# Kernel tuning notes

Measured on AMD Instinct MI355X. Metric: run time of the kernel, lower is better.

The kernel has to match this reference:

```python
import jax, jax.numpy as jnp
import numpy as np

B, N, D, H, FF, K, L = 8, 4096, 128, 8, 512, 16, 2
DH = D // H
EPS = 1e-5


def setup_inputs() -> dict:
    key = jax.random.key(0)
    ks = jax.random.split(key, 32)
    s = 0.02
    inp = {
        "x": jax.random.normal(ks[0], (B, N, 8), dtype=jnp.float32),
        "xyz_w": jax.random.normal(ks[1], (D, 3), jnp.float32) * s,
        "xyz_b": jnp.zeros((D,), jnp.float32),
        "ohe_w": jax.random.normal(ks[2], (D, 5), jnp.float32) * s,
        "ohe_b": jnp.zeros((D,), jnp.float32),
        # per-layer transformer params stacked on leading L axis
        "in_proj_w": jax.random.normal(ks[3], (L, 3 * D, D), jnp.float32) * s,
        "in_proj_b": jnp.zeros((L, 3 * D), jnp.float32),
        "out_proj_w": jax.random.normal(ks[4], (L, D, D), jnp.float32) * s,
        "out_proj_b": jnp.zeros((L, D), jnp.float32),
        "ln1_w": jnp.ones((L, D), jnp.float32),
        "ln1_b": jnp.zeros((L, D), jnp.float32),
        "lin1_w": jax.random.normal(ks[5], (L, FF, D), jnp.float32) * s,
        "lin1_b": jnp.zeros((L, FF), jnp.float32),
        "lin2_w": jax.random.normal(ks[6], (L, D, FF), jnp.float32) * s,
        "lin2_b": jnp.zeros((L, D), jnp.float32),
        "ln2_w": jnp.ones((L, D), jnp.float32),
        "ln2_b": jnp.zeros((L, D), jnp.float32),
        "fc1_w": jax.random.normal(ks[7], (FF, D), jnp.float32) * s,
        "fc1_b": jnp.zeros((FF,), jnp.float32),
        "fc2_w": jax.random.normal(ks[8], (1, FF), jnp.float32) * s,
        "fc2_b": jnp.zeros((1,), jnp.float32),
    }
    return inp


def _layer_norm(x, w, b):
    m = jnp.mean(x, -1, keepdims=True)
    v = jnp.mean((x - m) ** 2, -1, keepdims=True)
    return (x - m) * jax.lax.rsqrt(v + EPS) * w + b


def _knn_attention(xyz, feat):
    # squared euclidean distances preserve top-k ordering of cdist(p=2)
    d2 = jnp.sum((xyz[:, :, None, :] - xyz[:, None, :, :]) ** 2, -1)  # [B,N,N]
    _, idx = jax.lax.top_k(-d2, K + 1)  # ascending distance
    idx = idx[..., 1:]  # drop self -> [B,N,K]
    knn = jax.vmap(lambda f, i: f[i])(feat, idx)  # [B,N,K,D]
    scale = 1.0 / np.sqrt(D)
    scores = jnp.einsum('bnd,bnkd->bnk', feat, knn) * scale
    w = jax.nn.softmax(scores, -1)
    return jnp.einsum('bnk,bnkd->bnd', w, knn)


def _mha(x, in_w, in_b, out_w, out_b):
    qkv = x @ in_w.T + in_b  # [B,N,3D]
    q, k, v = jnp.split(qkv, 3, axis=-1)
    def heads(t):
        return t.reshape(B, N, H, DH).transpose(0, 2, 1, 3)  # [B,H,N,DH]
    q, k, v = heads(q), heads(k), heads(v)
    scores = jnp.einsum('bhqd,bhkd->bhqk', q, k) / np.sqrt(DH)
    a = jax.nn.softmax(scores, -1)
    o = jnp.einsum('bhqk,bhkd->bhqd', a, v).transpose(0, 2, 1, 3).reshape(B, N, D)
    return o @ out_w.T + out_b


def reference(x, xyz_w, xyz_b, ohe_w, ohe_b, in_proj_w, in_proj_b, out_proj_w,
              out_proj_b, ln1_w, ln1_b, lin1_w, lin1_b, lin2_w, lin2_b,
              ln2_w, ln2_b, fc1_w, fc1_b, fc2_w, fc2_b):
    xyz = x[:, :, :3]
    ohe = x[:, :, 3:8]
    feat = (xyz @ xyz_w.T + xyz_b) + (ohe @ ohe_w.T + ohe_b)  # [B,N,D]
    h = _knn_attention(xyz, feat)
    # post-norm TransformerEncoder (PyTorch default, relu, no dropout at eval)
    for l in range(L):
        a = _mha(h, in_proj_w[l], in_proj_b[l], out_proj_w[l], out_proj_b[l])
        h = _layer_norm(h + a, ln1_w[l], ln1_b[l])
        f = jax.nn.relu(h @ lin1_w[l].T + lin1_b[l]) @ lin2_w[l].T + lin2_b[l]
        h = _layer_norm(h + f, ln2_w[l], ln2_b[l])
    pooled = jnp.mean(h, axis=1)  # [B,D]
    out = jax.nn.sigmoid(jax.nn.relu(pooled @ fc1_w.T + fc1_b) @ fc2_w.T + fc2_b)
    return out
```

## Files before the change

### kernel.cpp

```cpp
#include <hip/hip_runtime.h>

#define Bq 8
#define Nq 4096
#define Dq 128
#define Hq 8
#define FFq 512
#define KNNq 16
#define Lq 2
#define DHq 16
#define EPSq 1e-5f

typedef _Float16 half4 __attribute__((ext_vector_type(4)));
typedef _Float16 half2t __attribute__((ext_vector_type(2)));
typedef float v4f __attribute__((ext_vector_type(4)));

static __device__ __forceinline__ half2t pkrtz(float a, float b) {
    return __builtin_bit_cast(half2t, __builtin_amdgcn_cvt_pkrtz(a, b));
}

__global__ void wcvt_kernel(const float* __restrict__ ipw, const float* __restrict__ opw,
                            const float* __restrict__ l1w, const float* __restrict__ l2w,
                            _Float16* __restrict__ wb) {
    int i = blockIdx.x * 256 + threadIdx.x;
    float v;
    if (i < 98304) v = ipw[i];
    else if (i < 131072) v = opw[i - 98304];
    else if (i < 262144) v = l1w[i - 131072];
    else v = l2w[i - 262144];
    wb[i] = (_Float16)v;
}

__global__ void feat_kernel(const float* __restrict__ x, const float* __restrict__ xyz_w,
                            const float* __restrict__ xyz_b, const float* __restrict__ ohe_w,
                            const float* __restrict__ ohe_b, _Float16* __restrict__ feat16) {
    int i = blockIdx.x * blockDim.x + threadIdx.x;
    if (i >= Bq * Nq * Dq) return;
    int d = i & 127;
    int t = i >> 7;
    const float* xr = x + (size_t)t * 8;
    float s = xyz_b[d] + ohe_b[d];
    s += xr[0] * xyz_w[d * 3 + 0] + xr[1] * xyz_w[d * 3 + 1] + xr[2] * xyz_w[d * 3 + 2];
    s += xr[3] * ohe_w[d * 5 + 0] + xr[4] * ohe_w[d * 5 + 1] + xr[5] * ohe_w[d * 5 + 2]
       + xr[6] * ohe_w[d * 5 + 3] + xr[7] * ohe_w[d * 5 + 4];
    feat16[i] = (_Float16)s;
}

__global__ __launch_bounds__(256) void knn_kernel(const float* __restrict__ x, int* __restrict__ idx) {
    __shared__ __attribute__((aligned(16))) float sxyz[Nq][4];
    __shared__ unsigned int md[256][16];
    int b = blockIdx.y;
    int tid = threadIdx.x;
    for (int p = tid; p < Nq; p += 256) {
        const float* xr = x + ((size_t)b * Nq + p) * 8;
        float4 v = make_float4(xr[0], xr[1], xr[2], 0.f);
        *(float4*)&sxyz[p][0] = v;
    }
    __syncthreads();
    int qi = tid >> 3;
    int part = tid & 7;
    int n = blockIdx.x * 32 + qi;
    float qx = sxyz[n][0], qy = sxyz[n][1], qz = sxyz[n][2];
    unsigned int bd[KNNq];
#pragma unroll
    for (int i = 0; i < KNNq; i++) bd[i] = 0xFFFFFFFFu;
    int j0 = part * 512;
    int rot = part * 2;
#pragma unroll 2
    for (int jj = 0; jj < 512; jj++) {
        int j = j0 + ((jj + rot) & 511);
        float4 p4 = *(const float4*)&sxyz[j][0];
        float dx = qx - p4.x, dy = qy - p4.y, dz = qz - p4.z;
        float d2 = fmaf(dx, dx, fmaf(dy, dy, dz * dz));
        unsigned int key = (__float_as_uint(d2) & 0xFFFFF000u) | (unsigned int)j;
        key = (j == n) ? 0xFFFFFFFFu : key;
#pragma unroll
        for (int i = 0; i < KNNq; i++) {
            unsigned int lo = bd[i] < key ? bd[i] : key;
            unsigned int hi = bd[i] < key ? key : bd[i];
            bd[i] = lo; key = hi;
        }
    }
#pragma unroll
    for (int i = 0; i < KNNq; i++) md[tid][i] = bd[i];
    __syncthreads();
    if (part == 0) {
        unsigned int pall = 0;
        int* op = idx + ((size_t)b * Nq + n) * KNNq;
        int base_row = qi * 8;
#pragma unroll
        for (int s = 0; s < KNNq; s++) {
            unsigned int best = 0xFFFFFFFFu; int bp = 0;
#pragma unroll
            for (int p2 = 0; p2 < 8; p2++) {
                unsigned int ptr = (pall >> (p2 * 4)) & 15u;
                unsigned int v = md[base_row + p2][ptr];
                if (v < best) { best = v; bp = p2; }
            }
            op[s] = (int)(best & 4095u);
            pall += (1u << (bp * 4));
        }
    }
}

__global__ __launch_bounds__(256, 4) void knn_attn_kernel(const _Float16* __restrict__ feat16,
                                                          const int* __restrict__ idx,
                                                          float* __restrict__ h,
                                                          _Float16* __restrict__ h16) {
    int wave = threadIdx.x >> 6;
    int lane = threadIdx.x & 63;
    int token = blockIdx.x * 4 + wave;
    int b = token >> 12;
    half2t fh = ((const half2t*)(feat16 + (size_t)token * Dq))[lane];
    float2 f = make_float2((float)fh[0], (float)fh[1]);
    const int* ip = idx + (size_t)token * KNNq;
    int jj[KNNq];
#pragma unroll
    for (int k = 0; k < KNNq; k++) jj[k] = ip[k];
    float2 g[KNNq];
#pragma unroll
    for (int k = 0; k < KNNq; k++) {
        half2t gh = ((const half2t*)(feat16 + (((size_t)b << 12) + jj[k]) * Dq))[lane];
        g[k] = make_float2((float)gh[0], (float)gh[1]);
    }
    float sc[KNNq];
#pragma unroll
    for (int k = 0; k < KNNq; k++) {
        float p = f.x * g[k].x + f.y * g[k].y;
#pragma unroll
        for (int m = 1; m < 64; m <<= 1) p += __shfl_xor(p, m);
        sc[k] = p * 0.088388347648318447f;
    }
    float mx = sc[0];
#pragma unroll
    for (int k = 1; k < KNNq; k++) mx = fmaxf(mx, sc[k]);
    float sum = 0.f;
#pragma unroll
    for (int k = 0; k < KNNq; k++) { sc[k] = __expf(sc[k] - mx); sum += sc[k]; }
    float inv = 1.f / sum;
    float o0 = 0.f, o1 = 0.f;
#pragma unroll
    for (int k = 0; k < KNNq; k++) { o0 += sc[k] * g[k].x; o1 += sc[k] * g[k].y; }
    o0 *= inv; o1 *= inv;
    ((float2*)(h + (size_t)token * Dq))[lane] = make_float2(o0, o1);
    ((half2t*)(h16 + (size_t)token * Dq))[lane] = pkrtz(o0, o1);
}

template <int MODE>
__global__ __launch_bounds__(256) void hgemm_kernel(const _Float16* __restrict__ A,
                                                    const _Float16* __restrict__ W,
                                                    const float* __restrict__ bias,
                                                    void* __restrict__ Cout,
                                                    int M, int Nc, int K) {
    int tid = threadIdx.x;
    int lane = tid & 63, w = tid >> 6;
    int l15 = lane & 15, l4 = lane >> 4;
    int m0 = blockIdx.y * 64 + w * 16;
    int n0 = blockIdx.x * 64;
    const _Float16* Ap = A + (size_t)(m0 + l15) * K + l4 * 4;
    const _Float16* Wp = W + (size_t)(n0 + l15) * K + l4 * 4;
    v4f acc[4] = {{0.f, 0.f, 0.f, 0.f}, {0.f, 0.f, 0.f, 0.f}, {0.f, 0.f, 0.f, 0.f}, {0.f, 0.f, 0.f, 0.f}};
    for (int ks = 0; ks < K; ks += 16) {
        half4 af = *(const half4*)(Ap + ks);
#pragma unroll
        for (int nt = 0; nt < 4; nt++) {
            half4 wf = *(const half4*)(Wp + (size_t)nt * 16 * K + ks);
            acc[nt] = __builtin_amdgcn_mfma_f32_16x16x16f16(wf, af, acc[nt], 0, 0, 0);
        }
    }
    int m = m0 + l15;
#pragma unroll
    for (int nt = 0; nt < 4; nt++) {
        int nb = n0 + nt * 16 + l4 * 4;
        float4 bv = *(const float4*)(bias + nb);
        float v0 = acc[nt][0] + bv.x, v1 = acc[nt][1] + bv.y;
        float v2 = acc[nt][2] + bv.z, v3 = acc[nt][3] + bv.w;
        if (MODE == 1) {
            v0 = fmaxf(v0, 0.f); v1 = fmaxf(v1, 0.f); v2 = fmaxf(v2, 0.f); v3 = fmaxf(v3, 0.f);
        }
        int n_base = n0 + nt * 16;
        int sel = n_base >> 7;
        if (MODE == 2 && sel == 0) {
            v0 *= 0.36067376f; v1 *= 0.36067376f; v2 *= 0.36067376f; v3 *= 0.36067376f;
        }
        half2t lo = pkrtz(v0, v1);
        half2t hi = pkrtz(v2, v3);
        half4 hv; hv[0] = lo[0]; hv[1] = lo[1]; hv[2] = hi[0]; hv[3] = hi[1];
        if (MODE == 1) {
            *(half4*)((_Float16*)Cout + (size_t)m * Nc + nb) = hv;
        } else {
            if (sel < 2) {
                int hh = (n_base >> 4) & 7;
                size_t base = (size_t)sel * (64ull * Nq * 16)
                            + ((size_t)((m >> 12) * 8 + hh)) * (Nq * 16)
                            + (size_t)(m & 4095) * 16 + l4 * 4;
                *(half4*)((_Float16*)Cout + base) = hv;
            } else {
                int hh = (n_base >> 4) & 7;
                size_t vb = 2ull * 64 * Nq * 16
                          + ((size_t)((m >> 12) * 8 + hh)) * (16 * Nq)
                          + (size_t)(m & 4095);
                _Float16* vp = (_Float16*)Cout + vb + (size_t)(l4 * 4) * Nq;
                vp[0 * Nq] = hv[0]; vp[1 * Nq] = hv[1]; vp[2 * Nq] = hv[2]; vp[3 * Nq] = hv[3];
            }
        }
    }
}

__global__ __launch_bounds__(256) void flash7_kernel(const _Float16* __restrict__ pk,
                                                     _Float16* __restrict__ out16) {
    __shared__ _Float16 Ks[2][64 * 20];
    __shared__ _Float16 Vs[2][16 * 66];
    int tid = threadIdx.x;
    int lane = tid & 63, w = tid >> 6;
    int bh = blockIdx.y;
    const _Float16* Qb = pk + (size_t)bh * (Nq * 16);
    const _Float16* Kb = pk + (size_t)(64 + bh) * (Nq * 16);
    const _Float16* Vt = pk + 2ull * 64 * Nq * 16 + (size_t)bh * (16 * Nq);
    int q0 = blockIdx.x * 64 + w * 16;
    int l15 = lane & 15, l4 = lane >> 4;

    half4 qf = *(const half4*)(Qb + (size_t)(q0 + l15) * 16 + l4 * 4);
    half4 ones; ones[0] = (_Float16)1.f; ones[1] = (_Float16)1.f; ones[2] = (_Float16)1.f; ones[3] = (_Float16)1.f;

    int sr = tid >> 2, sc = tid & 3;
    int vd = tid >> 4, vj = (tid & 15) * 4;
    const _Float16* Kg = Kb + (size_t)sr * 16 + sc * 4;
    const _Float16* Vg = Vt + (size_t)vd * Nq + vj;

    *(half4*)(Ks[0] + sr * 20 + sc * 4) = *(const half4*)(Kg);
    *(half4*)(Vs[0] + vd * 66 + vj) = *(const half4*)(Vg);
    __syncthreads();

    v4f o = {0.f, 0.f, 0.f, 0.f};
    v4f ls = {0.f, 0.f, 0.f, 0.f};

    for (int kt = 0; kt < Nq / 64; kt++) {
        int cur = kt & 1, nxt = cur ^ 1;
        if (kt < Nq / 64 - 1) {
            *(half4*)(Ks[nxt] + sr * 20 + sc * 4) = *(const half4*)(Kg + (size_t)(kt + 1) * 64 * 16);
            *(half4*)(Vs[nxt] + vd * 66 + vj) = *(const half4*)(Vg + (kt + 1) * 64);
        }
        v4f S[4];
#pragma unroll
        for (int g = 0; g < 4; g++) {
            half4 kf = *(const half4*)(Ks[cur] + (g * 16 + l15) * 20 + l4 * 4);
            S[g] = __builtin_amdgcn_mfma_f32_16x16x16f16(kf, qf, (v4f){0.f, 0.f, 0.f, 0.f}, 0, 0, 0);
        }
        half4 P[4];
#pragma unroll
        for (int g = 0; g < 4; g++) {
            float p0 = __builtin_amdgcn_exp2f(S[g][0]);
            float p1 = __builtin_amdgcn_exp2f(S[g][1]);
            float p2 = __builtin_amdgcn_exp2f(S[g][2]);
            float p3 = __builtin_amdgcn_exp2f(S[g][3]);
            half2t lo = pkrtz(p0, p1);
            half2t hi = pkrtz(p2, p3);
            P[g][0] = lo[0]; P[g][1] = lo[1]; P[g][2] = hi[0]; P[g][3] = hi[1];
        }
#pragma unroll
        for (int g = 0; g < 4; g++) {
            half4 vf = *(const half4*)(Vs[cur] + l15 * 66 + g * 16 + l4 * 4);
            o = __builtin_amdgcn_mfma_f32_16x16x16f16(vf, P[g], o, 0, 0, 0);
            ls = __builtin_amdgcn_mfma_f32_16x16x16f16(ones, P[g], ls, 0, 0, 0);
        }
        __syncthreads();
    }
    float inv = 1.f / ls[0];
    int row = q0 + l15;
    int b = bh >> 3, hh = bh & 7;
    half2t lo = pkrtz(o[0] * inv, o[1] * inv);
    half2t hi = pkrtz(o[2] * inv, o[3] * inv);
    half4 hv; hv[0] = lo[0]; hv[1] = lo[1]; hv[2] = hi[0]; hv[3] = hi[1];
    *(half4*)(out16 + ((size_t)(b * Nq + row)) * Dq + hh * 16 + l4 * 4) = hv;
}

__global__ __launch_bounds__(256) void hgemm_ln_kernel(const _Float16* __restrict__ A,
                                                       const _Float16* __restrict__ W,
                                                       const float* __restrict__ bias,
                                                       const float* __restrict__ lnw,
                                                       const float* __restrict__ lnb,
                                                       float* __restrict__ h,
                                                       _Float16* __restrict__ h16,
                                                       int K) {
    int tid = threadIdx.x;
    int lane = tid & 63, w = tid >> 6;
    int l15 = lane & 15, l4 = lane >> 4;
    int m0 = blockIdx.x * 64 + w * 16;
    const _Float16* Ap = A + (size_t)(m0 + l15) * K + l4 * 4;
    const _Float16* Wp = W + (size_t)l15 * K + l4 * 4;
    v4f acc[8] = {};
    for (int ks = 0; ks < K; ks += 16) {
        half4 af = *(const half4*)(Ap + ks);
#pragma unroll
        for (int nt = 0; nt < 8; nt++) {
            half4 wf = *(const half4*)(Wp + (size_t)nt * 16 * K + ks);
            acc[nt] = __builtin_amdgcn_mfma_f32_16x16x16f16(wf, af, acc[nt], 0, 0, 0);
        }
    }
    int m = m0 + l15;
    float x[8][4];
    float psum = 0.f;
#pragma unroll
    for (int nt = 0; nt < 8; nt++) {
        int nb = nt * 16 + l4 * 4;
        float4 bv = *(const float4*)(bias + nb);
        half4 rv = *(const half4*)(h16 + (size_t)m * Dq + nb);
        x[nt][0] = acc[nt][0] + bv.x + (float)rv[0];
        x[nt][1] = acc[nt][1] + bv.y + (float)rv[1];
        x[nt][2] = acc[nt][2] + bv.z + (float)rv[2];
        x[nt][3] = acc[nt][3] + bv.w + (float)rv[3];
        psum += (x[nt][0] + x[nt][1]) + (x[nt][2] + x[nt][3]);
    }
    psum += __shfl_xor(psum, 16);
    psum += __shfl_xor(psum, 32);
    float mean = psum * (1.f / 128.f);
    float vsum = 0.f;
#pragma unroll
    for (int nt = 0; nt < 8; nt++)
#pragma unroll
        for (int r = 0; r < 4; r++) {
            x[nt][r] -= mean;
            vsum += x[nt][r] * x[nt][r];
        }
    vsum += __shfl_xor(vsum, 16);
    vsum += __shfl_xor(vsum, 32);
    float inv = rsqrtf(vsum * (1.f / 128.f) + EPSq);
#pragma unroll
    for (int nt = 0; nt < 8; nt++) {
        int nb = nt * 16 + l4 * 4;
        float4 wv = *(const float4*)(lnw + nb);
        float4 bb = *(const float4*)(lnb + nb);
        float y0 = x[nt][0] * inv * wv.x + bb.x;
        float y1 = x[nt][1] * inv * wv.y + bb.y;
        float y2 = x[nt][2] * inv * wv.z + bb.z;
        float y3 = x[nt][3] * inv * wv.w + bb.w;
        *(float4*)(h + (size_t)m * Dq + nb) = make_float4(y0, y1, y2, y3);
        half2t lo = pkrtz(y0, y1);
        half2t hi = pkrtz(y2, y3);
        half4 hv2; hv2[0] = lo[0]; hv2[1] = lo[1]; hv2[2] = hi[0]; hv2[3] = hi[1];
        *(half4*)(h16 + (size_t)m * Dq + nb) = hv2;
    }
}

__global__ void pool_kernel(const float* __restrict__ h, float* __restrict__ part) {
    int c = blockIdx.x, b = blockIdx.y, d = threadIdx.x;
    const float* p = h + ((size_t)b * Nq + c * 256) * Dq + d;
    float s = 0.f;
    for (int n = 0; n < 256; n++) s += p[(size_t)n * Dq];
    part[((size_t)b * 16 + c) * Dq + d] = s;
}

__global__ __launch_bounds__(512) void head_kernel(const float* __restrict__ part,
                                                   const float* __restrict__ fc1_w, const float* __restrict__ fc1_b,
                                                   const float* __restrict__ fc2_w, const float* __restrict__ fc2_b,
                                                   float* __restrict__ out) {
    __shared__ float psh[Dq];
    __shared__ float red[512];
    int b = blockIdx.x, f = threadIdx.x;
    if (f < Dq) {
        float s = 0.f;
        for (int c = 0; c < 16; c++) s += part[((size_t)b * 16 + c) * Dq + f];
        psh[f] = s * (1.f / 4096.f);
    }
    __syncthreads();
    const float* wr = fc1_w + (size_t)f * Dq;
    float s = fc1_b[f];
    for (int d = 0; d < Dq; d++) s += psh[d] * wr[d];
    red[f] = fmaxf(s, 0.f) * fc2_w[f];
    __syncthreads();
    for (int st = 256; st > 0; st >>= 1) {
        if (f < st) red[f] += red[f + st];
        __syncthreads();
    }
    if (f == 0) out[b] = 1.f / (1.f + __expf(-(red[0] + fc2_b[0])));
}

extern "C" void kernel_launch(void* const* d_in, const int* in_sizes, int n_in,
                              void* d_out, int out_size, void* d_ws, size_t ws_size,
                              hipStream_t stream) {
    const float* x        = (const float*)d_in[0];
    const float* xyz_w    = (const float*)d_in[1];
    const float* xyz_b    = (const float*)d_in[2];
    const float* ohe_w    = (const float*)d_in[3];
    const float* ohe_b    = (const float*)d_in[4];
    const float* in_proj_w  = (const float*)d_in[5];
    const float* in_proj_b  = (const float*)d_in[6];
    const float* out_proj_w = (const float*)d_in[7];
    const float* out_proj_b = (const float*)d_in[8];
    const float* ln1_w    = (const float*)d_in[9];
    const float* ln1_b    = (const float*)d_in[10];
    const float* lin1_w   = (const float*)d_in[11];
    const float* lin1_b   = (const float*)d_in[12];
    const float* lin2_w   = (const float*)d_in[13];
    const float* lin2_b   = (const float*)d_in[14];
    const float* ln2_w    = (const float*)d_in[15];
    const float* ln2_b    = (const float*)d_in[16];
    const float* fc1_w    = (const float*)d_in[17];
    const float* fc1_b    = (const float*)d_in[18];
    const float* fc2_w    = (const float*)d_in[19];
    const float* fc2_b    = (const float*)d_in[20];
    float* outp = (float*)d_out;

    char* ws = (char*)d_ws;
    size_t off = 0;
    auto alloc = [&](size_t bytes) { void* p = ws + off; off += (bytes + 255) & ~255ULL; return p; };
    _Float16*  feat16 = (_Float16*)alloc((size_t)Bq * Nq * Dq * 2);
    float*     h      = (float*)alloc((size_t)Bq * Nq * Dq * 4);
    _Float16*  h16    = (_Float16*)alloc((size_t)Bq * Nq * Dq * 2);
    _Float16*  abuf16 = (_Float16*)alloc((size_t)Bq * Nq * Dq * 2);
    char*      bigu   = (char*)alloc((size_t)Bq * Nq * FFq * 2);
    _Float16*  wb     = (_Float16*)alloc(393216ull * 2);
    int*       idx    = (int*)alloc((size_t)Bq * Nq * KNNq * 4);
    float*     part   = (float*)alloc((size_t)Bq * 16 * Dq * 4);
    if (off > ws_size) return;
    _Float16* pkb   = (_Float16*)bigu;
    _Float16* big16 = (_Float16*)bigu;

    const _Float16* wip16 = wb;
    const _Float16* wop16 = wb + 98304;
    const _Float16* wl116 = wb + 131072;
    const _Float16* wl216 = wb + 262144;

    int M = Bq * Nq;

    wcvt_kernel<<<1536, 256, 0, stream>>>(in_proj_w, out_proj_w, lin1_w, lin2_w, wb);
    feat_kernel<<<(Bq * Nq * Dq + 255) / 256, 256, 0, stream>>>(x, xyz_w, xyz_b, ohe_w, ohe_b, feat16);
    knn_kernel<<<dim3(Nq / 32, Bq), 256, 0, stream>>>(x, idx);
    knn_attn_kernel<<<M / 4, 256, 0, stream>>>(feat16, idx, h, h16);

    for (int l = 0; l < Lq; l++) {
        hgemm_kernel<2><<<dim3(384 / 64, M / 64), 256, 0, stream>>>(
            h16, wip16 + (size_t)l * 384 * 128, in_proj_b + l * 384, pkb, M, 384, 128);
        flash7_kernel<<<dim3(Nq / 64, Bq * Hq), 256, 0, stream>>>(pkb, abuf16);
        hgemm_ln_kernel<<<M / 64, 256, 0, stream>>>(
            abuf16, wop16 + (size_t)l * 128 * 128, out_proj_b + l * 128,
            ln1_w + l * 128, ln1_b + l * 128, h, h16, 128);
        hgemm_kernel<1><<<dim3(512 / 64, M / 64), 256, 0, stream>>>(
            h16, wl116 + (size_t)l * 512 * 128, lin1_b + l * 512, big16, M, 512, 128);
        hgemm_ln_kernel<<<M / 64, 256, 0, stream>>>(
            big16, wl216 + (size_t)l * 128 * 512, lin2_b + l * 128,
            ln2_w + l * 128, ln2_b + l * 128, h, h16, 512);
    }

    pool_kernel<<<dim3(16, Bq), 128, 0, stream>>>(h, part);
    head_kernel<<<Bq, 512, 0, stream>>>(part, fc1_w, fc1_b, fc2_w, fc2_b, outp);
}
```

Before: 1.161 ms.

## Fuse FFN lin1, ReLU, lin2 and LayerNorm into one register-resident kernel

Adds an ffn_kernel where each wave computes lin1 plus ReLU for its 16 rows and keeps the 512-wide fp16 intermediate in registers. It then runs lin2, the residual add and LayerNorm in the same kernel. This removes the round trip of the large intermediate activation buffer through global memory and one kernel launch per layer. The workspace now allocates only the qkv pack buffer, and the unused ReLU path in hgemm_kernel is dropped. In exchange each wave holds many more VGPRs, which may lower occupancy, and it still streams both weight matrices from cache without LDS reuse.

```diff
diff --git a/kernel.cpp b/kernel.cpp
--- a/kernel.cpp
+++ b/kernel.cpp
@@ -174,9 +174,6 @@
         float4 bv = *(const float4*)(bias + nb);
         float v0 = acc[nt][0] + bv.x, v1 = acc[nt][1] + bv.y;
         float v2 = acc[nt][2] + bv.z, v3 = acc[nt][3] + bv.w;
-        if (MODE == 1) {
-            v0 = fmaxf(v0, 0.f); v1 = fmaxf(v1, 0.f); v2 = fmaxf(v2, 0.f); v3 = fmaxf(v3, 0.f);
-        }
         int n_base = n0 + nt * 16;
         int sel = n_base >> 7;
         if (MODE == 2 && sel == 0) {
@@ -185,23 +182,19 @@
         half2t lo = pkrtz(v0, v1);
         half2t hi = pkrtz(v2, v3);
         half4 hv; hv[0] = lo[0]; hv[1] = lo[1]; hv[2] = hi[0]; hv[3] = hi[1];
-        if (MODE == 1) {
-            *(half4*)((_Float16*)Cout + (size_t)m * Nc + nb) = hv;
+        if (sel < 2) {
+            int hh = (n_base >> 4) & 7;
+            size_t base = (size_t)sel * (64ull * Nq * 16)
+                        + ((size_t)((m >> 12) * 8 + hh)) * (Nq * 16)
+                        + (size_t)(m & 4095) * 16 + l4 * 4;
+            *(half4*)((_Float16*)Cout + base) = hv;
         } else {
-            if (sel < 2) {
-                int hh = (n_base >> 4) & 7;
-                size_t base = (size_t)sel * (64ull * Nq * 16)
-                            + ((size_t)((m >> 12) * 8 + hh)) * (Nq * 16)
-                            + (size_t)(m & 4095) * 16 + l4 * 4;
-                *(half4*)((_Float16*)Cout + base) = hv;
-            } else {
-                int hh = (n_base >> 4) & 7;
-                size_t vb = 2ull * 64 * Nq * 16
-                          + ((size_t)((m >> 12) * 8 + hh)) * (16 * Nq)
-                          + (size_t)(m & 4095);
-                _Float16* vp = (_Float16*)Cout + vb + (size_t)(l4 * 4) * Nq;
-                vp[0 * Nq] = hv[0]; vp[1 * Nq] = hv[1]; vp[2 * Nq] = hv[2]; vp[3 * Nq] = hv[3];
-            }
+            int hh = (n_base >> 4) & 7;
+            size_t vb = 2ull * 64 * Nq * 16
+                      + ((size_t)((m >> 12) * 8 + hh)) * (16 * Nq)
+                      + (size_t)(m & 4095);
+            _Float16* vp = (_Float16*)Cout + vb + (size_t)(l4 * 4) * Nq;
+            vp[0 * Nq] = hv[0]; vp[1 * Nq] = hv[1]; vp[2 * Nq] = hv[2]; vp[3 * Nq] = hv[3];
         }
     }
 }
@@ -309,6 +302,100 @@
         x[nt][1] = acc[nt][1] + bv.y + (float)rv[1];
         x[nt][2] = acc[nt][2] + bv.z + (float)rv[2];
         x[nt][3] = acc[nt][3] + bv.w + (float)rv[3];
+        psum += (x[nt][0] + x[nt][1]) + (x[nt][2] + x[nt][3]);
+    }
+    psum += __shfl_xor(psum, 16);
+    psum += __shfl_xor(psum, 32);
+    float mean = psum * (1.f / 128.f);
+    float vsum = 0.f;
+#pragma unroll
+    for (int nt = 0; nt < 8; nt++)
+#pragma unroll
+        for (int r = 0; r < 4; r++) {
+            x[nt][r] -= mean;
+            vsum += x[nt][r] * x[nt][r];
+        }
+    vsum += __shfl_xor(vsum, 16);
+    vsum += __shfl_xor(vsum, 32);
+    float inv = rsqrtf(vsum * (1.f / 128.f) + EPSq);
+#pragma unroll
+    for (int nt = 0; nt < 8; nt++) {
+        int nb = nt * 16 + l4 * 4;
+        float4 wv = *(const float4*)(lnw + nb);
+        float4 bb = *(const float4*)(lnb + nb);
+        float y0 = x[nt][0] * inv * wv.x + bb.x;
+        float y1 = x[nt][1] * inv * wv.y + bb.y;
+        float y2 = x[nt][2] * inv * wv.z + bb.z;
+        float y3 = x[nt][3] * inv * wv.w + bb.w;
+        *(float4*)(h + (size_t)m * Dq + nb) = make_float4(y0, y1, y2, y3);
+        half2t lo = pkrtz(y0, y1);
+        half2t hi = pkrtz(y2, y3);
+        half4 hv2; hv2[0] = lo[0]; hv2[1] = lo[1]; hv2[2] = hi[0]; hv2[3] = hi[1];
+        *(half4*)(h16 + (size_t)m * Dq + nb) = hv2;
+    }
+}
+
+__global__ __launch_bounds__(256) void ffn_kernel(const _Float16* __restrict__ h16in,
+                                                  const _Float16* __restrict__ W1,
+                                                  const float* __restrict__ b1,
+                                                  const _Float16* __restrict__ W2,
+                                                  const float* __restrict__ b2,
+                                                  const float* __restrict__ lnw,
+                                                  const float* __restrict__ lnb,
+                                                  float* __restrict__ h,
+                                                  _Float16* __restrict__ h16) {
+    int tid = threadIdx.x;
+    int lane = tid & 63, w = tid >> 6;
+    int l15 = lane & 15, l4 = lane >> 4;
+    int m0 = blockIdx.x * 64 + w * 16;
+    int m = m0 + l15;
+    const _Float16* Ap = h16in + (size_t)m * Dq + l4 * 4;
+    half4 afr[8];
+#pragma unroll
+    for (int t = 0; t < 8; t++) afr[t] = *(const half4*)(Ap + t * 16);
+    half4 mid[32];
+#pragma unroll
+    for (int c = 0; c < 8; c++) {
+        v4f acc[4] = {};
+#pragma unroll
+        for (int t = 0; t < 8; t++) {
+#pragma unroll
+            for (int nt = 0; nt < 4; nt++) {
+                half4 wf = *(const half4*)(W1 + (size_t)(c * 64 + nt * 16 + l15) * 128 + t * 16 + l4 * 4);
+                acc[nt] = __builtin_amdgcn_mfma_f32_16x16x16f16(wf, afr[t], acc[nt], 0, 0, 0);
+            }
+        }
+#pragma unroll
+        for (int nt = 0; nt < 4; nt++) {
+            float4 bv = *(const float4*)(b1 + c * 64 + nt * 16 + l4 * 4);
+            float v0 = fmaxf(acc[nt][0] + bv.x, 0.f);
+            float v1 = fmaxf(acc[nt][1] + bv.y, 0.f);
+            float v2 = fmaxf(acc[nt][2] + bv.z, 0.f);
+            float v3 = fmaxf(acc[nt][3] + bv.w, 0.f);
+            half2t lo = pkrtz(v0, v1), hi = pkrtz(v2, v3);
+            half4 hv; hv[0] = lo[0]; hv[1] = lo[1]; hv[2] = hi[0]; hv[3] = hi[1];
+            mid[c * 4 + nt] = hv;
+        }
+    }
+    v4f acc8[8] = {};
+#pragma unroll 4
+    for (int t = 0; t < 32; t++) {
+#pragma unroll
+        for (int nt = 0; nt < 8; nt++) {
+            half4 wf = *(const half4*)(W2 + (size_t)(nt * 16 + l15) * 512 + t * 16 + l4 * 4);
+            acc8[nt] = __builtin_amdgcn_mfma_f32_16x16x16f16(wf, mid[t], acc8[nt], 0, 0, 0);
+        }
+    }
+    float x[8][4];
+    float psum = 0.f;
+#pragma unroll
+    for (int nt = 0; nt < 8; nt++) {
+        int nb = nt * 16 + l4 * 4;
+        float4 bv = *(const float4*)(b2 + nb);
+        x[nt][0] = acc8[nt][0] + bv.x + (float)afr[nt][0];
+        x[nt][1] = acc8[nt][1] + bv.y + (float)afr[nt][1];
+        x[nt][2] = acc8[nt][2] + bv.z + (float)afr[nt][2];
+        x[nt][3] = acc8[nt][3] + bv.w + (float)afr[nt][3];
         psum += (x[nt][0] + x[nt][1]) + (x[nt][2] + x[nt][3]);
     }
     psum += __shfl_xor(psum, 16);
@@ -408,13 +495,11 @@
     float*     h      = (float*)alloc((size_t)Bq * Nq * Dq * 4);
     _Float16*  h16    = (_Float16*)alloc((size_t)Bq * Nq * Dq * 2);
     _Float16*  abuf16 = (_Float16*)alloc((size_t)Bq * Nq * Dq * 2);
-    char*      bigu   = (char*)alloc((size_t)Bq * Nq * FFq * 2);
+    _Float16*  pkb    = (_Float16*)alloc(3ull * 64 * Nq * 16 * 2);
     _Float16*  wb     = (_Float16*)alloc(393216ull * 2);
     int*       idx    = (int*)alloc((size_t)Bq * Nq * KNNq * 4);
     float*     part   = (float*)alloc((size_t)Bq * 16 * Dq * 4);
     if (off > ws_size) return;
-    _Float16* pkb   = (_Float16*)bigu;
-    _Float16* big16 = (_Float16*)bigu;
 
     const _Float16* wip16 = wb;
     const _Float16* wop16 = wb + 98304;
@@ -435,11 +520,10 @@
         hgemm_ln_kernel<<<M / 64, 256, 0, stream>>>(
             abuf16, wop16 + (size_t)l * 128 * 128, out_proj_b + l * 128,
             ln1_w + l * 128, ln1_b + l * 128, h, h16, 128);
-        hgemm_kernel<1><<<dim3(512 / 64, M / 64), 256, 0, stream>>>(
-            h16, wl116 + (size_t)l * 512 * 128, lin1_b + l * 512, big16, M, 512, 128);
-        hgemm_ln_kernel<<<M / 64, 256, 0, stream>>>(
-            big16, wl216 + (size_t)l * 128 * 512, lin2_b + l * 128,
-            ln2_w + l * 128, ln2_b + l * 128, h, h16, 512);
+        ffn_kernel<<<M / 64, 256, 0, stream>>>(
+            h16, wl116 + (size_t)l * 512 * 128, lin1_b + l * 512,
+            wl216 + (size_t)l * 128 * 512, lin2_b + l * 128,
+            ln2_w + l * 128, ln2_b + l * 128, h, h16);
     }
 
     pool_kernel<<<dim3(16, Bq), 128, 0, stream>>>(h, part);
```

Result: no change. 1.148 ms (-1.1%).
